# Performance work log

Hardware: AMD Instinct MI355X
Metric: run time of the kernel (lower is better)

Reference implementation:

```python
import jax, jax.numpy as jnp
import numpy as np
from jax import lax

ALPHA_LO = float(np.exp(-1.0 / 5.0))
ALPHA_HI = float(np.exp(-1.0 / 25.0))
THRESHOLD = 1.0


def setup_inputs() -> dict:
    key = jax.random.key(0)
    k1, k2, k3, k4, k5 = jax.random.split(key, 5)
    B, T, I, H = 64, 1024, 512, 512
    x = jax.random.normal(k1, (B, T, I), dtype=jnp.float32)
    # kaiming-uniform-like small init for Linear weight
    bound = 1.0 / np.sqrt(I)
    W = jax.random.uniform(k2, (H, I), minval=-bound, maxval=bound, dtype=jnp.float32)
    alpha = ALPHA_LO + jax.random.uniform(k3, (H,), dtype=jnp.float32) * (ALPHA_HI - ALPHA_LO)
    u0 = jax.random.uniform(k4, (B, H), dtype=jnp.float32)
    s0 = jax.random.uniform(k5, (B, H), dtype=jnp.float32)
    return {"x": x, "W": W, "alpha": alpha, "u0": u0, "s0": s0}


def reference(x, W, alpha, u0, s0):
    # x: [B, T, I], W: [H, I] (torch Linear layout), alpha/u0/s0 over H
    al = jnp.clip(alpha, ALPHA_LO, ALPHA_HI)  # [H]
    Wx = jnp.einsum('bti,hi->bth', x, W)      # [B, T, H]

    def step(carry, wx_t):
        u, s = carry
        u = al * (u - s) + (1.0 - al) * wx_t
        s = (u - THRESHOLD > 0).astype(wx_t.dtype)
        return (u, s), s

    _, spikes = lax.scan(step, (u0, s0), jnp.swapaxes(Wx, 0, 1))  # [T, B, H]
    return jnp.swapaxes(spikes, 0, 1)  # [B, T, H]
```

## Files before the change

kernel.cpp:

```cpp
#include <hip/hip_runtime.h>
#include <hip/hip_bf16.h>


#define ALPHA_LO_F ((float)0.8187307530779818)
#define ALPHA_HI_F ((float)0.9607894391523232)

typedef float v2f __attribute__((ext_vector_type(2)));

#define TM 128
#define TN 128
#define TK 16
__global__ __launch_bounds__(256) void gemm_nt_f32(
    const float* __restrict__ A,
    const float* __restrict__ B,
    float* __restrict__ C,
    int M, int N, int K)
{
    __shared__ float As[TK][TM];
    __shared__ float Bs[TK][TN];

    const int tid = threadIdx.x;
    const int m0  = blockIdx.y * TM;
    const int n0  = blockIdx.x * TN;

    const int lrow = tid >> 1;
    const int lkq  = (tid & 1) * 8;

    const int tm = tid >> 4;
    const int tn = tid & 15;

    v2f acc[8][4] = {};

    const float* Arow = A + (size_t)(m0 + lrow) * K + lkq;
    const float* Brow = B + (size_t)(n0 + lrow) * K + lkq;

    for (int k0 = 0; k0 < K; k0 += TK) {
        float4 av0 = *(const float4*)(Arow + k0);
        float4 av1 = *(const float4*)(Arow + k0 + 4);
        float4 bv0 = *(const float4*)(Brow + k0);
        float4 bv1 = *(const float4*)(Brow + k0 + 4);
        As[lkq + 0][lrow] = av0.x;  As[lkq + 1][lrow] = av0.y;
        As[lkq + 2][lrow] = av0.z;  As[lkq + 3][lrow] = av0.w;
        As[lkq + 4][lrow] = av1.x;  As[lkq + 5][lrow] = av1.y;
        As[lkq + 6][lrow] = av1.z;  As[lkq + 7][lrow] = av1.w;
        Bs[lkq + 0][lrow] = bv0.x;  Bs[lkq + 1][lrow] = bv0.y;
        Bs[lkq + 2][lrow] = bv0.z;  Bs[lkq + 3][lrow] = bv0.w;
        Bs[lkq + 4][lrow] = bv1.x;  Bs[lkq + 5][lrow] = bv1.y;
        Bs[lkq + 6][lrow] = bv1.z;  Bs[lkq + 7][lrow] = bv1.w;
        __syncthreads();

        #pragma unroll
        for (int k = 0; k < TK; ++k) {
            const float* Ak = &As[k][tm * 8];
            const float* Bk = &Bs[k][tn * 8];
            float4 a0 = *(const float4*)(Ak);
            float4 a1 = *(const float4*)(Ak + 4);
            float4 b0 = *(const float4*)(Bk);
            float4 b1 = *(const float4*)(Bk + 4);
            v2f bb[4];
            bb[0] = (v2f){b0.x, b0.y};  bb[1] = (v2f){b0.z, b0.w};
            bb[2] = (v2f){b1.x, b1.y};  bb[3] = (v2f){b1.z, b1.w};
            float a[8] = {a0.x, a0.y, a0.z, a0.w, a1.x, a1.y, a1.z, a1.w};
            #pragma unroll
            for (int i = 0; i < 8; ++i) {
                v2f ai = (v2f){a[i], a[i]};
                #pragma unroll
                for (int jv = 0; jv < 4; ++jv)
                    acc[i][jv] = __builtin_elementwise_fma(ai, bb[jv], acc[i][jv]);
            }
        }
        __syncthreads();
    }

    #pragma unroll
    for (int i = 0; i < 8; ++i) {
        float* Crow = C + (size_t)(m0 + tm * 8 + i) * N + n0 + tn * 8;
        float4 v0, v1;
        v0.x = acc[i][0].x; v0.y = acc[i][0].y; v0.z = acc[i][1].x; v0.w = acc[i][1].y;
        v1.x = acc[i][2].x; v1.y = acc[i][2].y; v1.z = acc[i][3].x; v1.w = acc[i][3].y;
        *(float4*)(Crow)     = v0;
        *(float4*)(Crow + 4) = v1;
    }
}

#define PF 32
__global__ __launch_bounds__(64) void lif_scan(
    float* __restrict__ buf,
    const float* __restrict__ alpha,
    const float* __restrict__ u0,
    const float* __restrict__ s0,
    int B, int T, int H)
{
    const int h = blockIdx.x * blockDim.x + threadIdx.x;
    const int b = blockIdx.y;
    if (h >= H) return;

    float al = alpha[h];
    al = fminf(fmaxf(al, ALPHA_LO_F), ALPHA_HI_F);
    const float one_m_al = 1.0f - al;

    float u = u0[(size_t)b * H + h];
    float s = s0[(size_t)b * H + h];

    const size_t sH = (size_t)H;
    size_t idx = (size_t)b * T * H + h;

    float cur[PF], nxt[PF];
    #pragma unroll
    for (int j = 0; j < PF; ++j) cur[j] = buf[idx + (size_t)j * sH];

    for (int t0 = 0; t0 < T; t0 += PF) {
        const size_t nidx = idx + (size_t)PF * sH;
        if (t0 + PF < T) {
            #pragma unroll
            for (int j = 0; j < PF; ++j) nxt[j] = buf[nidx + (size_t)j * sH];
        }
        #pragma unroll
        for (int j = 0; j < PF; ++j) {
            u = al * (u - s) + one_m_al * cur[j];
            s = (u - 1.0f > 0.0f) ? 1.0f : 0.0f;
            cur[j] = s;
        }
        #pragma unroll
        for (int j = 0; j < PF; ++j) buf[idx + (size_t)j * sH] = cur[j];
        #pragma unroll
        for (int j = 0; j < PF; ++j) cur[j] = nxt[j];
        idx = nidx;
    }
}

extern "C" void kernel_launch(void* const* d_in, const int* in_sizes, int n_in,
                              void* d_out, int out_size, void* d_ws, size_t ws_size,
                              hipStream_t stream) {
    const float* x     = (const float*)d_in[0];
    const float* W     = (const float*)d_in[1];
    const float* alpha = (const float*)d_in[2];
    const float* u0    = (const float*)d_in[3];
    const float* s0    = (const float*)d_in[4];
    float* out = (float*)d_out;

    const int H = in_sizes[2];
    const int I = in_sizes[1] / H;
    const int B = in_sizes[3] / H;
    const int T = in_sizes[0] / (B * I);
    const int M = B * T;

    dim3 grid1(H / TN, M / TM);
    gemm_nt_f32<<<grid1, 256, 0, stream>>>(x, W, out, M, H, I);

    dim3 grid2((H + 63) / 64, B);
    lif_scan<<<grid2, 64, 0, stream>>>(out, alpha, u0, s0, B, T, H);
}
```

Before: 624.2 us.

## Double-buffer GEMM tiles and warp-specialize LIF scan with async LDS prefetch

The GEMM now double-buffers its shared-memory tiles, so the global loads for the next K-tile are issued before compute on the current tile and only one barrier runs per iteration. It also splits each thread's B columns into two halves 64 apart, which changes the LDS read pattern and the output store layout. The scan kernel becomes warp-specialized: four producer waves stream time chunks into a 4-deep LDS ring with global_load_lds, while one consumer wave runs the recurrence and writes the spikes out. The aim is to hide the latency of the serial scan's strided global loads, at the cost of hand-written vmcnt and barrier choreography that assumes T and H divide evenly.

```diff
diff --git a/kernel.cpp b/kernel.cpp
--- a/kernel.cpp
+++ b/kernel.cpp
@@ -1,5 +1,4 @@
 #include <hip/hip_runtime.h>
-#include <hip/hip_bf16.h>
 
 
 #define ALPHA_LO_F ((float)0.8187307530779818)
@@ -16,8 +15,8 @@
     float* __restrict__ C,
     int M, int N, int K)
 {
-    __shared__ float As[TK][TM];
-    __shared__ float Bs[TK][TN];
+    __shared__ float As[2][TK][TM];
+    __shared__ float Bs[2][TK][TN];
 
     const int tid = threadIdx.x;
     const int m0  = blockIdx.y * TM;
@@ -34,29 +33,43 @@
     const float* Arow = A + (size_t)(m0 + lrow) * K + lkq;
     const float* Brow = B + (size_t)(n0 + lrow) * K + lkq;
 
-    for (int k0 = 0; k0 < K; k0 += TK) {
-        float4 av0 = *(const float4*)(Arow + k0);
-        float4 av1 = *(const float4*)(Arow + k0 + 4);
-        float4 bv0 = *(const float4*)(Brow + k0);
-        float4 bv1 = *(const float4*)(Brow + k0 + 4);
-        As[lkq + 0][lrow] = av0.x;  As[lkq + 1][lrow] = av0.y;
-        As[lkq + 2][lrow] = av0.z;  As[lkq + 3][lrow] = av0.w;
-        As[lkq + 4][lrow] = av1.x;  As[lkq + 5][lrow] = av1.y;
-        As[lkq + 6][lrow] = av1.z;  As[lkq + 7][lrow] = av1.w;
-        Bs[lkq + 0][lrow] = bv0.x;  Bs[lkq + 1][lrow] = bv0.y;
-        Bs[lkq + 2][lrow] = bv0.z;  Bs[lkq + 3][lrow] = bv0.w;
-        Bs[lkq + 4][lrow] = bv1.x;  Bs[lkq + 5][lrow] = bv1.y;
-        Bs[lkq + 6][lrow] = bv1.z;  Bs[lkq + 7][lrow] = bv1.w;
-        __syncthreads();
+    float4 av0 = *(const float4*)(Arow);
+    float4 av1 = *(const float4*)(Arow + 4);
+    float4 bv0 = *(const float4*)(Brow);
+    float4 bv1 = *(const float4*)(Brow + 4);
+    {
+        float va[8] = {av0.x, av0.y, av0.z, av0.w, av1.x, av1.y, av1.z, av1.w};
+        float vb[8] = {bv0.x, bv0.y, bv0.z, bv0.w, bv1.x, bv1.y, bv1.z, bv1.w};
+        #pragma unroll
+        for (int j = 0; j < 8; ++j) {
+            As[0][lkq + j][lrow] = va[j];
+            Bs[0][lkq + j][lrow] = vb[j];
+        }
+    }
+    __syncthreads();
+
+    const int NT = K / TK;
+    int cur = 0;
+    for (int kt = 0; kt < NT; ++kt) {
+        const bool pf = (kt + 1 < NT);
+        if (pf) {
+            const float* An = Arow + (size_t)(kt + 1) * TK;
+            const float* Bn = Brow + (size_t)(kt + 1) * TK;
+            av0 = *(const float4*)(An);
+            av1 = *(const float4*)(An + 4);
+            bv0 = *(const float4*)(Bn);
+            bv1 = *(const float4*)(Bn + 4);
+        }
 
         #pragma unroll
         for (int k = 0; k < TK; ++k) {
-            const float* Ak = &As[k][tm * 8];
-            const float* Bk = &Bs[k][tn * 8];
+            const float* Ak  = &As[cur][k][tm * 8];
+            const float* Bk0 = &Bs[cur][k][tn * 4];
+            const float* Bk1 = &Bs[cur][k][64 + tn * 4];
             float4 a0 = *(const float4*)(Ak);
             float4 a1 = *(const float4*)(Ak + 4);
-            float4 b0 = *(const float4*)(Bk);
-            float4 b1 = *(const float4*)(Bk + 4);
+            float4 b0 = *(const float4*)(Bk0);
+            float4 b1 = *(const float4*)(Bk1);
             v2f bb[4];
             bb[0] = (v2f){b0.x, b0.y};  bb[1] = (v2f){b0.z, b0.w};
             bb[2] = (v2f){b1.x, b1.y};  bb[3] = (v2f){b1.z, b1.w};
@@ -69,63 +82,115 @@
                     acc[i][jv] = __builtin_elementwise_fma(ai, bb[jv], acc[i][jv]);
             }
         }
+
+        if (pf) {
+            const int nb = cur ^ 1;
+            float va[8] = {av0.x, av0.y, av0.z, av0.w, av1.x, av1.y, av1.z, av1.w};
+            float vb[8] = {bv0.x, bv0.y, bv0.z, bv0.w, bv1.x, bv1.y, bv1.z, bv1.w};
+            #pragma unroll
+            for (int j = 0; j < 8; ++j) {
+                As[nb][lkq + j][lrow] = va[j];
+                Bs[nb][lkq + j][lrow] = vb[j];
+            }
+        }
         __syncthreads();
+        cur ^= 1;
     }
 
     #pragma unroll
     for (int i = 0; i < 8; ++i) {
-        float* Crow = C + (size_t)(m0 + tm * 8 + i) * N + n0 + tn * 8;
+        float* Crow = C + (size_t)(m0 + tm * 8 + i) * N + n0;
         float4 v0, v1;
         v0.x = acc[i][0].x; v0.y = acc[i][0].y; v0.z = acc[i][1].x; v0.w = acc[i][1].y;
         v1.x = acc[i][2].x; v1.y = acc[i][2].y; v1.z = acc[i][3].x; v1.w = acc[i][3].y;
-        *(float4*)(Crow)     = v0;
-        *(float4*)(Crow + 4) = v1;
+        *(float4*)(Crow + tn * 4)      = v0;
+        *(float4*)(Crow + 64 + tn * 4) = v1;
     }
 }
 
-#define PF 32
-__global__ __launch_bounds__(64) void lif_scan(
+#define C_T  64
+#define NBUF 4
+
+__global__ __launch_bounds__(320) void lif_scan(
     float* __restrict__ buf,
     const float* __restrict__ alpha,
     const float* __restrict__ u0,
     const float* __restrict__ s0,
     int B, int T, int H)
 {
-    const int h = blockIdx.x * blockDim.x + threadIdx.x;
-    const int b = blockIdx.y;
-    if (h >= H) return;
-
-    float al = alpha[h];
-    al = fminf(fmaxf(al, ALPHA_LO_F), ALPHA_HI_F);
-    const float one_m_al = 1.0f - al;
-
-    float u = u0[(size_t)b * H + h];
-    float s = s0[(size_t)b * H + h];
-
-    const size_t sH = (size_t)H;
-    size_t idx = (size_t)b * T * H + h;
-
-    float cur[PF], nxt[PF];
-    #pragma unroll
-    for (int j = 0; j < PF; ++j) cur[j] = buf[idx + (size_t)j * sH];
-
-    for (int t0 = 0; t0 < T; t0 += PF) {
-        const size_t nidx = idx + (size_t)PF * sH;
-        if (t0 + PF < T) {
-            #pragma unroll
-            for (int j = 0; j < PF; ++j) nxt[j] = buf[nidx + (size_t)j * sH];
-        }
-        #pragma unroll
-        for (int j = 0; j < PF; ++j) {
-            u = al * (u - s) + one_m_al * cur[j];
-            s = (u - 1.0f > 0.0f) ? 1.0f : 0.0f;
-            cur[j] = s;
-        }
-        #pragma unroll
-        for (int j = 0; j < PF; ++j) buf[idx + (size_t)j * sH] = cur[j];
-        #pragma unroll
-        for (int j = 0; j < PF; ++j) cur[j] = nxt[j];
-        idx = nidx;
+    __shared__ float S[NBUF][C_T][64];
+
+    const int tid  = threadIdx.x;
+    const int wid  = tid >> 6;
+    const int lane = tid & 63;
+    const int b    = blockIdx.y;
+    const int h0   = blockIdx.x * 64;
+    const int nch  = T / C_T;
+
+    float* base = buf + (size_t)b * T * H + h0;
+
+    if (wid == 0) {
+        const int h = h0 + lane;
+        float al = alpha[h];
+        al = fminf(fmaxf(al, ALPHA_LO_F), ALPHA_HI_F);
+        const float oma = 1.0f - al;
+        float u = u0[(size_t)b * H + h];
+        float s = s0[(size_t)b * H + h];
+
+        for (int j = 0; j < nch; ++j) {
+            asm volatile("s_barrier" ::: "memory");
+            const float* Sj = &S[j & (NBUF - 1)][0][0] + lane;
+            float* orow = base + (size_t)j * C_T * H + lane;
+            for (int tb = 0; tb < C_T; tb += 16) {
+                float w[16];
+                #pragma unroll
+                for (int tt = 0; tt < 16; ++tt)
+                    w[tt] = Sj[(tb + tt) * 64];
+                #pragma unroll
+                for (int tt = 0; tt < 16; ++tt) {
+                    u = al * (u - s) + oma * w[tt];
+                    s = (u - 1.0f > 0.0f) ? 1.0f : 0.0f;
+                    w[tt] = s;
+                }
+                #pragma unroll
+                for (int tt = 0; tt < 16; ++tt)
+                    orow[(size_t)(tb + tt) * H] = w[tt];
+            }
+            asm volatile("s_waitcnt lgkmcnt(0)" ::: "memory");
+            asm volatile("s_barrier" ::: "memory");
+        }
+    } else {
+        const int lw = wid - 1;
+
+        #define ISSUE_CHUNK(c)                                                  \
+            {                                                                   \
+                const int cc = (c);                                             \
+                char* sb = (char*)&S[cc & (NBUF - 1)][0][0];                    \
+                _Pragma("unroll")                                               \
+                for (int q = 0; q < 4; ++q) {                                   \
+                    const int i = lw + 4 * q;                                   \
+                    const int t = cc * C_T + i * 4 + (lane >> 4);               \
+                    const float* g = base + (size_t)t * H + (lane & 15) * 4;    \
+                    __builtin_amdgcn_global_load_lds(                           \
+                        (const __attribute__((address_space(1))) unsigned int*)g, \
+                        (__attribute__((address_space(3))) unsigned int*)(sb + i * 1024), \
+                        16, 0, 0);                                              \
+                }                                                               \
+            }
+
+        for (int c = 0; c < NBUF - 1; ++c) ISSUE_CHUNK(c)
+
+        for (int j = 0; j < nch; ++j) {
+            const int c = j + NBUF - 1;
+            if (c < nch) ISSUE_CHUNK(c)
+            if (j < nch - 3)       asm volatile("s_waitcnt vmcnt(12)" ::: "memory");
+            else if (j == nch - 3) asm volatile("s_waitcnt vmcnt(8)"  ::: "memory");
+            else if (j == nch - 2) asm volatile("s_waitcnt vmcnt(4)"  ::: "memory");
+            else                   asm volatile("s_waitcnt vmcnt(0)"  ::: "memory");
+            asm volatile("s_barrier" ::: "memory");
+            asm volatile("s_barrier" ::: "memory");
+        }
+        #undef ISSUE_CHUNK
     }
 }
 
@@ -148,6 +213,6 @@
     dim3 grid1(H / TN, M / TM);
     gemm_nt_f32<<<grid1, 256, 0, stream>>>(x, W, out, M, H, I);
 
-    dim3 grid2((H + 63) / 64, B);
-    lif_scan<<<grid2, 64, 0, stream>>>(out, alpha, u0, s0, B, T, H);
+    dim3 grid2(H / 64, B);
+    lif_scan<<<grid2, 320, 0, stream>>>(out, alpha, u0, s0, B, T, H);
 }
```

Measured after the change: 787.3 us. 1.26x slower.

## Fuse GEMM and LIF scan into one kernel with per-batch time chunking

Applied to the files above, without the earlier changes.

Replaces the separate fp32 GEMM and LIF scan kernels with one fused kernel. Each block owns one batch and 64 hidden units and walks the time axis in 128-step chunks. Each chunk computes its Wx tile into shared memory, then 64 threads run the recurrence and write spikes with nontemporal stores. This removes the global round trip of the intermediate Wx tensor and a second launch. The costs are a narrower GEMM tile, only 512 blocks, and a serial scan phase where most threads sit idle.

```diff
diff --git a/kernel.cpp b/kernel.cpp
--- a/kernel.cpp
+++ b/kernel.cpp
@@ -1,131 +1,113 @@
 #include <hip/hip_runtime.h>
-#include <hip/hip_bf16.h>
 
 
 #define ALPHA_LO_F ((float)0.8187307530779818)
 #define ALPHA_HI_F ((float)0.9607894391523232)
 
-typedef float v2f __attribute__((ext_vector_type(2)));
+typedef float v4f __attribute__((ext_vector_type(4)));
 
-#define TM 128
-#define TN 128
-#define TK 16
-__global__ __launch_bounds__(256) void gemm_nt_f32(
-    const float* __restrict__ A,
-    const float* __restrict__ B,
-    float* __restrict__ C,
-    int M, int N, int K)
+#define FTM 128
+#define FTN 64
+#define FTK 16
+
+__global__ __launch_bounds__(256) void lif_fused(
+    const float* __restrict__ x,
+    const float* __restrict__ W,
+    const float* __restrict__ alpha,
+    const float* __restrict__ u0,
+    const float* __restrict__ s0,
+    float* __restrict__ out,
+    int Bn, int T, int I, int H)
 {
-    __shared__ float As[TK][TM];
-    __shared__ float Bs[TK][TN];
+    __shared__ float As[FTK][FTM];
+    __shared__ float Bs[FTK][FTN];
+    __shared__ float Wxs[FTM][FTN];
 
     const int tid = threadIdx.x;
-    const int m0  = blockIdx.y * TM;
-    const int n0  = blockIdx.x * TN;
+    const int h0  = blockIdx.x * FTN;
+    const int b   = blockIdx.y;
 
     const int lrow = tid >> 1;
     const int lkq  = (tid & 1) * 8;
+    const int brow = tid >> 2;
+    const int bkq  = (tid & 3) * 4;
 
     const int tm = tid >> 4;
     const int tn = tid & 15;
 
-    v2f acc[8][4] = {};
+    float u = 0.0f, s = 0.0f, al = 0.0f, oma = 0.0f;
+    if (tid < FTN) {
+        float a_ = alpha[h0 + tid];
+        a_ = fminf(fmaxf(a_, ALPHA_LO_F), ALPHA_HI_F);
+        al = a_;  oma = 1.0f - a_;
+        u = u0[(size_t)b * H + h0 + tid];
+        s = s0[(size_t)b * H + h0 + tid];
+    }
 
-    const float* Arow = A + (size_t)(m0 + lrow) * K + lkq;
-    const float* Brow = B + (size_t)(n0 + lrow) * K + lkq;
+    const float* Wrow = W + (size_t)(h0 + brow) * I + bkq;
 
-    for (int k0 = 0; k0 < K; k0 += TK) {
-        float4 av0 = *(const float4*)(Arow + k0);
-        float4 av1 = *(const float4*)(Arow + k0 + 4);
-        float4 bv0 = *(const float4*)(Brow + k0);
-        float4 bv1 = *(const float4*)(Brow + k0 + 4);
-        As[lkq + 0][lrow] = av0.x;  As[lkq + 1][lrow] = av0.y;
-        As[lkq + 2][lrow] = av0.z;  As[lkq + 3][lrow] = av0.w;
-        As[lkq + 4][lrow] = av1.x;  As[lkq + 5][lrow] = av1.y;
-        As[lkq + 6][lrow] = av1.z;  As[lkq + 7][lrow] = av1.w;
-        Bs[lkq + 0][lrow] = bv0.x;  Bs[lkq + 1][lrow] = bv0.y;
-        Bs[lkq + 2][lrow] = bv0.z;  Bs[lkq + 3][lrow] = bv0.w;
-        Bs[lkq + 4][lrow] = bv1.x;  Bs[lkq + 5][lrow] = bv1.y;
-        Bs[lkq + 6][lrow] = bv1.z;  Bs[lkq + 7][lrow] = bv1.w;
+    for (int t0 = 0; t0 < T; t0 += FTM) {
+        const float* Arow = x + ((size_t)b * T + t0 + lrow) * I + lkq;
+        float acc[8][4] = {};
+
+        for (int k0 = 0; k0 < I; k0 += FTK) {
+            float4 av0 = *(const float4*)(Arow + k0);
+            float4 av1 = *(const float4*)(Arow + k0 + 4);
+            float4 bv  = *(const float4*)(Wrow + k0);
+            As[lkq + 0][lrow] = av0.x;  As[lkq + 1][lrow] = av0.y;
+            As[lkq + 2][lrow] = av0.z;  As[lkq + 3][lrow] = av0.w;
+            As[lkq + 4][lrow] = av1.x;  As[lkq + 5][lrow] = av1.y;
+            As[lkq + 6][lrow] = av1.z;  As[lkq + 7][lrow] = av1.w;
+            Bs[bkq + 0][brow] = bv.x;   Bs[bkq + 1][brow] = bv.y;
+            Bs[bkq + 2][brow] = bv.z;   Bs[bkq + 3][brow] = bv.w;
+            __syncthreads();
+
+            #pragma unroll
+            for (int k = 0; k < FTK; ++k) {
+                const float* Ak = &As[k][tm * 8];
+                const float* Bk = &Bs[k][tn * 4];
+                float4 a0 = *(const float4*)(Ak);
+                float4 a1 = *(const float4*)(Ak + 4);
+                float4 b0 = *(const float4*)(Bk);
+                float a[8]  = {a0.x, a0.y, a0.z, a0.w, a1.x, a1.y, a1.z, a1.w};
+                float bb[4] = {b0.x, b0.y, b0.z, b0.w};
+                #pragma unroll
+                for (int i = 0; i < 8; ++i) {
+                    #pragma unroll
+                    for (int j = 0; j < 4; ++j)
+                        acc[i][j] = __builtin_fmaf(a[i], bb[j], acc[i][j]);
+                }
+            }
+            __syncthreads();
+        }
+
+        #pragma unroll
+        for (int i = 0; i < 8; ++i) {
+            v4f v;
+            v.x = acc[i][0]; v.y = acc[i][1]; v.z = acc[i][2]; v.w = acc[i][3];
+            *(v4f*)(&Wxs[tm * 8 + i][tn * 4]) = v;
+        }
         __syncthreads();
 
-        #pragma unroll
-        for (int k = 0; k < TK; ++k) {
-            const float* Ak = &As[k][tm * 8];
-            const float* Bk = &Bs[k][tn * 8];
-            float4 a0 = *(const float4*)(Ak);
-            float4 a1 = *(const float4*)(Ak + 4);
-            float4 b0 = *(const float4*)(Bk);
-            float4 b1 = *(const float4*)(Bk + 4);
-            v2f bb[4];
-            bb[0] = (v2f){b0.x, b0.y};  bb[1] = (v2f){b0.z, b0.w};
-            bb[2] = (v2f){b1.x, b1.y};  bb[3] = (v2f){b1.z, b1.w};
-            float a[8] = {a0.x, a0.y, a0.z, a0.w, a1.x, a1.y, a1.z, a1.w};
-            #pragma unroll
-            for (int i = 0; i < 8; ++i) {
-                v2f ai = (v2f){a[i], a[i]};
+        if (tid < FTN) {
+            float* orow = out + ((size_t)b * T + t0) * H + h0 + tid;
+            for (int tb = 0; tb < FTM; tb += 16) {
+                float w[16];
                 #pragma unroll
-                for (int jv = 0; jv < 4; ++jv)
-                    acc[i][jv] = __builtin_elementwise_fma(ai, bb[jv], acc[i][jv]);
+                for (int q = 0; q < 16; ++q)
+                    w[q] = Wxs[tb + q][tid];
+                #pragma unroll
+                for (int q = 0; q < 16; ++q) {
+                    u = al * (u - s) + oma * w[q];
+                    s = (u - 1.0f > 0.0f) ? 1.0f : 0.0f;
+                    w[q] = s;
+                }
+                #pragma unroll
+                for (int q = 0; q < 16; ++q)
+                    __builtin_nontemporal_store(w[q], orow + (size_t)(tb + q) * H);
             }
         }
         __syncthreads();
-    }
-
-    #pragma unroll
-    for (int i = 0; i < 8; ++i) {
-        float* Crow = C + (size_t)(m0 + tm * 8 + i) * N + n0 + tn * 8;
-        float4 v0, v1;
-        v0.x = acc[i][0].x; v0.y = acc[i][0].y; v0.z = acc[i][1].x; v0.w = acc[i][1].y;
-        v1.x = acc[i][2].x; v1.y = acc[i][2].y; v1.z = acc[i][3].x; v1.w = acc[i][3].y;
-        *(float4*)(Crow)     = v0;
-        *(float4*)(Crow + 4) = v1;
-    }
-}
-
-#define PF 32
-__global__ __launch_bounds__(64) void lif_scan(
-    float* __restrict__ buf,
-    const float* __restrict__ alpha,
-    const float* __restrict__ u0,
-    const float* __restrict__ s0,
-    int B, int T, int H)
-{
-    const int h = blockIdx.x * blockDim.x + threadIdx.x;
-    const int b = blockIdx.y;
-    if (h >= H) return;
-
-    float al = alpha[h];
-    al = fminf(fmaxf(al, ALPHA_LO_F), ALPHA_HI_F);
-    const float one_m_al = 1.0f - al;
-
-    float u = u0[(size_t)b * H + h];
-    float s = s0[(size_t)b * H + h];
-
-    const size_t sH = (size_t)H;
-    size_t idx = (size_t)b * T * H + h;
-
-    float cur[PF], nxt[PF];
-    #pragma unroll
-    for (int j = 0; j < PF; ++j) cur[j] = buf[idx + (size_t)j * sH];
-
-    for (int t0 = 0; t0 < T; t0 += PF) {
-        const size_t nidx = idx + (size_t)PF * sH;
-        if (t0 + PF < T) {
-            #pragma unroll
-            for (int j = 0; j < PF; ++j) nxt[j] = buf[nidx + (size_t)j * sH];
-        }
-        #pragma unroll
-        for (int j = 0; j < PF; ++j) {
-            u = al * (u - s) + one_m_al * cur[j];
-            s = (u - 1.0f > 0.0f) ? 1.0f : 0.0f;
-            cur[j] = s;
-        }
-        #pragma unroll
-        for (int j = 0; j < PF; ++j) buf[idx + (size_t)j * sH] = cur[j];
-        #pragma unroll
-        for (int j = 0; j < PF; ++j) cur[j] = nxt[j];
-        idx = nidx;
     }
 }
 
@@ -143,11 +125,7 @@
     const int I = in_sizes[1] / H;
     const int B = in_sizes[3] / H;
     const int T = in_sizes[0] / (B * I);
-    const int M = B * T;
 
-    dim3 grid1(H / TN, M / TM);
-    gemm_nt_f32<<<grid1, 256, 0, stream>>>(x, W, out, M, H, I);
-
-    dim3 grid2((H + 63) / 64, B);
-    lif_scan<<<grid2, 64, 0, stream>>>(out, alpha, u0, s0, B, T, H);
+    dim3 grid(H / FTN, B);
+    lif_fused<<<grid, 256, 0, stream>>>(x, W, alpha, u0, s0, out, B, T, I, H);
 }
```

Result: slower. 740.9 us (+18.7%).
